# Performance work log

Hardware: AMD Instinct MI355X
Metric: run time of the kernel (lower is better)

The kernel has to match this reference:

```python
import jax, jax.numpy as jnp
from jax import lax
import numpy as np


def _fps(xyz, M):
    # Farthest point sampling: sequential over M steps, vectorized over batch.
    B, N, _ = xyz.shape
    def body(carry, _):
        dists, far = carry                       # dists:[B,N], far:[B]
        c = xyz[jnp.arange(B), far]              # [B,3] current centroid
        d = jnp.sum((xyz - c[:, None, :]) ** 2, axis=-1)
        dists = jnp.minimum(dists, d)
        nxt = jnp.argmax(dists, axis=-1).astype(jnp.int32)
        return (dists, nxt), far
    init = (jnp.full((B, N), 1e10, xyz.dtype), jnp.zeros((B,), jnp.int32))
    _, inds = lax.scan(body, init, None, length=M)
    return inds.T                                # [B, M]


def _ball_query(xyz, new_xyz, radius, K):
    # For each centroid pick first K point indices within radius; pad with first hit.
    N = xyz.shape[1]
    d2 = jnp.sum((new_xyz[:, :, None, :] - xyz[:, None, :, :]) ** 2, axis=-1)  # [B,M,N]
    ids = jnp.where(d2 <= radius * radius, jnp.arange(N)[None, None, :], N)
    ids = jnp.sort(ids, axis=-1)[..., :K]        # [B,M,K]
    return jnp.where(ids == N, ids[..., :1], ids)


_gather = jax.vmap(lambda p, i: p[i])            # p:[N,C], i:[M,K] -> [M,K,C]


def _mlp(x, layers):
    # Shared per-point MLP (1x1 conv + ReLU chain); BN omitted as in source head.
    for w, b in layers:
        x = jax.nn.relu(jnp.einsum('bmkc,cd->bmkd', x, w) + b)
    return x


def _sa(xyz, points, M, radius, K, layers):
    # Set-abstraction: FPS -> ball query -> group (centered xyz ++ feats) -> MLP -> max over K.
    fi = _fps(xyz, M)                                        # [B,M]
    new_xyz = jnp.take_along_axis(xyz, fi[..., None], axis=1)  # [B,M,3]
    gi = _ball_query(xyz, new_xyz, radius, K)                # [B,M,K]
    g_xyz = _gather(xyz, gi) - new_xyz[:, :, None, :]        # [B,M,K,3]
    g = jnp.concatenate([g_xyz, _gather(points, gi)], axis=-1)
    return new_xyz, jnp.max(_mlp(g, layers), axis=2)         # [B,M,Cout]


def _forward(xyz, points,
             w1a, b1a, w1b, b1b, w1c, b1c,
             w2a, b2a, w2b, b2b, w2c, b2c,
             w3a, b3a, w3b, b3b, w3c, b3c,
             lin1_w, lin2_w, cls_w, cls_b):
    B = xyz.shape[0]
    x1, f1 = _sa(xyz, points, 512, 0.2, 32, [(w1a, b1a), (w1b, b1b), (w1c, b1c)])
    x2, f2 = _sa(x1, f1, 128, 0.4, 64, [(w2a, b2a), (w2b, b2b), (w2c, b2c)])
    # group_all: single group containing all 128 points, feats = [xyz ++ points] (259 ch)
    g = jnp.concatenate([x2, f2], axis=-1)[:, None]           # [B,1,128,259]
    f3 = jnp.max(_mlp(g, [(w3a, b3a), (w3b, b3b), (w3c, b3c)]), axis=2)  # [B,1,1024]
    net = f3.reshape(B, -1)
    net = jax.nn.relu(net @ lin1_w)   # linear1 (no bias) + ReLU; dropout=identity (eval)
    net = jax.nn.relu(net @ lin2_w)
    return net @ cls_w + cls_b


def setup_inputs() -> dict:
    key = jax.random.key(0)
    ks = iter(jax.random.split(key, 40))
    B, N, NC = 32, 1024, 40
    inp = {}
    inp['xyz'] = jax.random.uniform(next(ks), (B, N, 3), jnp.float32, -1.0, 1.0)
    inp['points'] = jax.random.normal(next(ks), (B, N, 3), jnp.float32)
    def lin(cin, cout):
        w = jax.random.normal(next(ks), (cin, cout), jnp.float32) / np.float32(np.sqrt(cin))
        return w, jnp.zeros((cout,), jnp.float32)
    dims = {'1': [(6, 64), (64, 64), (64, 128)],
            '2': [(131, 128), (128, 128), (128, 256)],
            '3': [(259, 256), (256, 512), (512, 1024)]}
    for s, layer_dims in dims.items():
        for tag, (ci, co) in zip('abc', layer_dims):
            w, b = lin(ci, co)
            inp['w%s%s' % (s, tag)] = w
            inp['b%s%s' % (s, tag)] = b
    inp['lin1_w'] = jax.random.normal(next(ks), (1024, 512), jnp.float32) / np.float32(32.0)
    inp['lin2_w'] = jax.random.normal(next(ks), (512, 256), jnp.float32) / np.float32(np.sqrt(512))
    inp['cls_w'] = jax.random.normal(next(ks), (256, NC), jnp.float32) / np.float32(16.0)
    inp['cls_b'] = jnp.zeros((NC,), jnp.float32)
    return inp


def reference(xyz, points,
              w1a, b1a, w1b, b1b, w1c, b1c,
              w2a, b2a, w2b, b2b, w2c, b2c,
              w3a, b3a, w3b, b3b, w3c, b3c,
              lin1_w, lin2_w, cls_w, cls_b):
    return _forward(xyz, points,
                    w1a, b1a, w1b, b1b, w1c, b1c,
                    w2a, b2a, w2b, b2b, w2c, b2c,
                    w3a, b3a, w3b, b3b, w3c, b3c,
                    lin1_w, lin2_w, cls_w, cls_b)
```

## Files before the change

### kernel.cpp

```cpp
#include <hip/hip_runtime.h>

#define DEVFN __device__ __forceinline__

static inline int ceil_div(int a, int b) { return (a + b - 1) / b; }

typedef __attribute__((ext_vector_type(8))) short         bf16x8;
typedef __attribute__((ext_vector_type(4))) float         f32x4;
typedef __attribute__((ext_vector_type(8))) unsigned short u16x8;

DEVFN unsigned short f2bf(float x) {
    unsigned u = __float_as_uint(x);
    unsigned r = ((u >> 16) & 1u) + 0x7fffu;
    return (unsigned short)((u + r) >> 16);
}
DEVFN float bf2f(unsigned short h) { return __uint_as_float(((unsigned)h) << 16); }

template<int CTRL>
DEVFN double dpp_max_step(double v)
{
    int lo = __double2loint(v), hi = __double2hiint(v);
    int tlo = __builtin_amdgcn_update_dpp(lo, lo, CTRL, 0xF, 0xF, false);
    int thi = __builtin_amdgcn_update_dpp(hi, hi, CTRL, 0xF, 0xF, false);
    return fmax(v, __hiloint2double(thi, tlo));
}

template<int N>
__global__ __launch_bounds__(64) void fps_kernel(const float* __restrict__ xyz, int M,
                                                 int* __restrict__ out_idx,
                                                 float* __restrict__ nxout)
{
    constexpr int PPL = N / 64;
    int b = blockIdx.x, lane = threadIdx.x;
    __shared__ float4 sp[N];
    const float* p = xyz + (size_t)b * N * 3;
    float px[PPL], py[PPL], pz[PPL], dd[PPL];
    unsigned lo[PPL];
    #pragma unroll
    for (int j = 0; j < PPL; ++j) {
        int idx = lane + 64 * j;
        px[j] = p[idx*3+0]; py[j] = p[idx*3+1]; pz[j] = p[idx*3+2];
        sp[idx] = make_float4(px[j], py[j], pz[j], 0.f);
        dd[j] = 1e10f;
        lo[j] = ~(unsigned)idx;
    }
    __syncthreads();
    int far = 0;
    for (int s = 0; s < M; ++s) {
        float4 c4 = sp[far];
        if (lane == 0) {
            out_idx[(size_t)b*M + s] = far;
            nxout[((size_t)b*M + s)*3 + 0] = c4.x;
            nxout[((size_t)b*M + s)*3 + 1] = c4.y;
            nxout[((size_t)b*M + s)*3 + 2] = c4.z;
        }
        double cand[PPL];
        #pragma unroll
        for (int j = 0; j < PPL; ++j) {
            float dx = __fsub_rn(px[j], c4.x);
            float dy = __fsub_rn(py[j], c4.y);
            float dz = __fsub_rn(pz[j], c4.z);
            float d  = __fadd_rn(__fadd_rn(__fmul_rn(dx,dx), __fmul_rn(dy,dy)),
                                 __fmul_rn(dz,dz));
            float nd = fminf(dd[j], d);
            dd[j] = nd;
            cand[j] = __hiloint2double(__float_as_int(nd), (int)lo[j]);
        }
        #pragma unroll
        for (int st = PPL/2; st > 0; st >>= 1)
            #pragma unroll
            for (int j = 0; j < PPL; ++j)
                if (j < st) cand[j] = fmax(cand[j], cand[j + st]);
        double v = cand[0];
        v = dpp_max_step<0xB1>(v);
        v = dpp_max_step<0x4E>(v);
        v = dpp_max_step<0x124>(v);
        v = dpp_max_step<0x128>(v);
        v = dpp_max_step<0x142>(v);
        v = dpp_max_step<0x143>(v);
        int wlo = __builtin_amdgcn_readlane(__double2loint(v), 63);
        far = (int)(~(unsigned)wlo);
    }
}

__global__ void ballquery_kernel(const float* __restrict__ xyz,
                                 const float* __restrict__ new_xyz,
                                 int* __restrict__ gi,
                                 int B, int N, int M, int K, float r2)
{
    int t = blockIdx.x * blockDim.x + threadIdx.x;
    if (t >= B * M) return;
    int b = t / M;
    const float* p = xyz + (size_t)b * N * 3;
    float cx = new_xyz[t*3+0], cy = new_xyz[t*3+1], cz = new_xyz[t*3+2];
    int* out = gi + (size_t)t * K;
    int cnt = 0, first = 0;
    bool havefirst = false;
    for (int i = 0; i < N; ++i) {
        float dx = __fsub_rn(p[i*3+0], cx);
        float dy = __fsub_rn(p[i*3+1], cy);
        float dz = __fsub_rn(p[i*3+2], cz);
        float d  = __fadd_rn(__fadd_rn(__fmul_rn(dx,dx), __fmul_rn(dy,dy)),
                             __fmul_rn(dz,dz));
        if (d <= r2) {
            if (!havefirst) { first = i; havefirst = true; }
            out[cnt++] = i;
            if (cnt == K) break;
        }
    }
    for (; cnt < K; ++cnt) out[cnt] = first;
}

DEVFN float f4_elem(const float4& v, int u) {
    return u == 0 ? v.x : u == 1 ? v.y : u == 2 ? v.z : v.w;
}

__global__ void wsplit_kernel(const float* __restrict__ w,
                              unsigned short* __restrict__ wh,
                              unsigned short* __restrict__ wl,
                              int CItot, int CO, int CIpad, int ro)
{
    int t = blockIdx.x * 256 + threadIdx.x;
    if (t >= CIpad * CO) return;
    int co = t / CIpad, ci = t % CIpad;
    int src = ci + ro;
    float v = (src < CItot) ? w[(size_t)src * CO + co] : 0.f;
    unsigned short h = f2bf(v);
    wh[t] = h;
    wl[t] = f2bf(v - bf2f(h));
}

template<int CF, int CO, int KPTS>
__global__ __launch_bounds__(256) void sa_l1_kernel(
    const float* __restrict__ xyz, const float* __restrict__ feats,
    const float* __restrict__ new_xyz, const int* __restrict__ gi,
    const float* __restrict__ w, const float* __restrict__ bias,
    unsigned short* __restrict__ oh, unsigned short* __restrict__ ol,
    int N, int M, int row0)
{
    constexpr int WCH = CO / 4;
    const int lane = threadIdx.x & 63;
    const int wv   = __builtin_amdgcn_readfirstlane(threadIdx.x >> 6);
    const int rl   = blockIdx.x * 64 + lane;
    const int row  = row0 + rl;
    const int cent = row / KPTS;
    const int b    = cent / M;
    const int idx  = gi[row];
    const float* pp  = xyz + ((size_t)b*N + idx)*3;
    const float* cc3 = new_xyz + (size_t)cent*3;
    float a0 = __fsub_rn(pp[0], cc3[0]);
    float a1 = __fsub_rn(pp[1], cc3[1]);
    float a2 = __fsub_rn(pp[2], cc3[2]);
    const float* frow = feats + ((size_t)b*N + idx)*CF;
    const float* wcol = w + wv*WCH;
    const float* bcol = bias + wv*WCH;
    float acc[WCH];
    #pragma unroll
    for (int j = 0; j < WCH; ++j) acc[j] = bcol[j];
    #pragma unroll
    for (int j = 0; j < WCH; ++j) acc[j] += a0 * wcol[0*CO + j];
    #pragma unroll
    for (int j = 0; j < WCH; ++j) acc[j] += a1 * wcol[1*CO + j];
    #pragma unroll
    for (int j = 0; j < WCH; ++j) acc[j] += a2 * wcol[2*CO + j];
    constexpr int CF4 = CF & ~3;
    #pragma unroll 2
    for (int cc = 0; cc < CF4; cc += 4) {
        float4 a4 = *(const float4*)(frow + cc);
        #pragma unroll
        for (int u = 0; u < 4; ++u) {
            float a = f4_elem(a4, u);
            #pragma unroll
            for (int j = 0; j < WCH; ++j)
                acc[j] += a * wcol[(size_t)(3 + cc + u)*CO + j];
        }
    }
    #pragma unroll
    for (int f = CF4; f < CF; ++f) {
        float a = frow[f];
        #pragma unroll
        for (int j = 0; j < WCH; ++j)
            acc[j] += a * wcol[(size_t)(3 + f)*CO + j];
    }
    #pragma unroll
    for (int j8 = 0; j8 < WCH; j8 += 8) {
        u16x8 hv, lv;
        #pragma unroll
        for (int u = 0; u < 8; ++u) {
            float v = fmaxf(acc[j8+u], 0.f);
            unsigned short h = f2bf(v);
            hv[u] = (unsigned short)h;
            lv[u] = f2bf(v - bf2f(h));
        }
        size_t o = (size_t)rl*CO + wv*WCH + j8;
        *(u16x8*)(&oh[o]) = hv;
        *(u16x8*)(&ol[o]) = lv;
    }
}

template<int CI, int CO, int NTILE, int MROW, int KPTS, int OUTMODE>
__global__ __launch_bounds__(256) void mfma_layer_kernel(
    const unsigned short* __restrict__ ah, const unsigned short* __restrict__ al,
    const unsigned short* __restrict__ wh, const unsigned short* __restrict__ wl,
    const float* __restrict__ bias,
    unsigned short* __restrict__ oh, unsigned short* __restrict__ ol,
    float* __restrict__ ofp, int rowbase)
{
    constexpr int KT = CI / 32;
    static_assert(KT * MROW <= 18, "A-preload register budget");
    __shared__ float partial[4][OUTMODE >= 2 ? MROW : 1][OUTMODE >= 2 ? 16*NTILE : 1];
    const int wid  = threadIdx.x >> 6;
    const int lane = threadIdx.x & 63;
    const int m    = lane & 15;
    const int kg   = lane >> 4;
    const int blockrow = blockIdx.x * (64 * MROW);
    const int colbase  = blockIdx.y * (16 * NTILE);
    bf16x8 Ahf[MROW * KT], Alf[MROW * KT];
    #pragma unroll
    for (int t = 0; t < MROW; ++t) {
        const unsigned short* arh =
            ah + (size_t)(blockrow + t*64 + wid*16 + m) * CI + kg * 8;
        const unsigned short* arl =
            al + (size_t)(blockrow + t*64 + wid*16 + m) * CI + kg * 8;
        #pragma unroll
        for (int kt = 0; kt < KT; ++kt) {
            Ahf[t*KT + kt] = *(const bf16x8*)(arh + kt*32);
            Alf[t*KT + kt] = *(const bf16x8*)(arl + kt*32);
        }
    }
    #pragma unroll
    for (int nt = 0; nt < NTILE; ++nt) {
        f32x4 acc[MROW];
        #pragma unroll
        for (int t = 0; t < MROW; ++t) acc[t] = (f32x4){0.f, 0.f, 0.f, 0.f};
        const unsigned short* wbh = wh + (size_t)(colbase + nt*16 + m) * CI + kg * 8;
        const unsigned short* wbl = wl + (size_t)(colbase + nt*16 + m) * CI + kg * 8;
        #pragma unroll
        for (int kt = 0; kt < KT; ++kt) {
            bf16x8 Bh = *(const bf16x8*)(wbh + kt*32);
            bf16x8 Bl = *(const bf16x8*)(wbl + kt*32);
            #pragma unroll
            for (int t = 0; t < MROW; ++t) {
                acc[t] = __builtin_amdgcn_mfma_f32_16x16x32_bf16(Ahf[t*KT+kt], Bh, acc[t], 0, 0, 0);
                acc[t] = __builtin_amdgcn_mfma_f32_16x16x32_bf16(Ahf[t*KT+kt], Bl, acc[t], 0, 0, 0);
                acc[t] = __builtin_amdgcn_mfma_f32_16x16x32_bf16(Alf[t*KT+kt], Bh, acc[t], 0, 0, 0);
            }
        }
        int dcol = colbase + nt*16 + m;
        float bv = bias[dcol];
        #pragma unroll
        for (int t = 0; t < MROW; ++t) {
            float v[4];
            #pragma unroll
            for (int r = 0; r < 4; ++r) v[r] = fmaxf(acc[t][r] + bv, 0.f);
            if constexpr (OUTMODE == 0) {
                #pragma unroll
                for (int r = 0; r < 4; ++r) {
                    size_t o = (size_t)(blockrow + t*64 + wid*16 + kg*4 + r) * CO + dcol;
                    unsigned short h = f2bf(v[r]);
                    oh[o] = h;
                    ol[o] = f2bf(v[r] - bf2f(h));
                }
            } else if constexpr (OUTMODE == 1) {
                #pragma unroll
                for (int r = 0; r < 4; ++r)
                    ofp[(size_t)(blockrow + t*64 + wid*16 + kg*4 + r) * CO + dcol] = v[r];
            } else {
                float mx = fmaxf(fmaxf(v[0], v[1]), fmaxf(v[2], v[3]));
                mx = fmaxf(mx, __shfl_xor(mx, 16));
                mx = fmaxf(mx, __shfl_xor(mx, 32));
                if (lane < 16) partial[wid][t][nt*16 + m] = mx;
            }
        }
    }
    if constexpr (OUTMODE >= 2) {
        __syncthreads();
        for (int c = threadIdx.x; c < 16*NTILE; c += 256) {
            #pragma unroll
            for (int t = 0; t < MROW; ++t) {
                if constexpr (KPTS == 64) {
                    float mx = fmaxf(fmaxf(partial[0][t][c], partial[1][t][c]),
                                     fmaxf(partial[2][t][c], partial[3][t][c]));
                    int cent = (rowbase + blockrow) / 64 + t;
                    if constexpr (OUTMODE == 2) {
                        ofp[(size_t)cent*CO + colbase + c] = mx;
                    } else {
                        size_t o = (size_t)cent*CO + colbase + c;
                        unsigned short h = f2bf(mx);
                        oh[o] = h; ol[o] = f2bf(mx - bf2f(h));
                    }
                } else {
                    int cent0 = (rowbase + blockrow) / 32 + t*2;
                    float v0 = fmaxf(partial[0][t][c], partial[1][t][c]);
                    float v1 = fmaxf(partial[2][t][c], partial[3][t][c]);
                    if constexpr (OUTMODE == 2) {
                        ofp[(size_t)cent0*CO + colbase + c]     = v0;
                        ofp[(size_t)(cent0+1)*CO + colbase + c] = v1;
                    } else {
                        size_t o0 = (size_t)cent0*CO + colbase + c;
                        size_t o1 = (size_t)(cent0+1)*CO + colbase + c;
                        unsigned short h0 = f2bf(v0), h1 = f2bf(v1);
                        oh[o0] = h0; ol[o0] = f2bf(v0 - bf2f(h0));
                        oh[o1] = h1; ol[o1] = f2bf(v1 - bf2f(h1));
                    }
                }
            }
        }
    }
}

template<int NTILE, int MROW>
__global__ __launch_bounds__(256) void mfma_sa2l1_kernel(
    const float* __restrict__ sxyz,
    const float* __restrict__ cxyz,
    const int* __restrict__ gi,
    const unsigned short* __restrict__ f1h, const unsigned short* __restrict__ f1l,
    const float* __restrict__ w,
    const unsigned short* __restrict__ wh, const unsigned short* __restrict__ wl,
    const float* __restrict__ bias,
    unsigned short* __restrict__ oh, unsigned short* __restrict__ ol,
    int rowbase)
{
    constexpr int CI = 128, CO = 128, KT = 4, KPTS = 64, M = 128, N = 512;
    const int wid  = threadIdx.x >> 6;
    const int lane = threadIdx.x & 63;
    const int m    = lane & 15;
    const int kg   = lane >> 4;
    const int blockrow = blockIdx.x * (64 * MROW);
    const int colbase  = blockIdx.y * (16 * NTILE);
    bf16x8 Ahf[MROW * KT], Alf[MROW * KT];
    #pragma unroll
    for (int t = 0; t < MROW; ++t) {
        int grow = rowbase + blockrow + t*64 + wid*16 + m;
        int cent = grow / KPTS;
        int b    = cent / M;
        int idx  = gi[grow];
        const unsigned short* arh = f1h + ((size_t)b*N + idx) * CI + kg * 8;
        const unsigned short* arl = f1l + ((size_t)b*N + idx) * CI + kg * 8;
        #pragma unroll
        for (int kt = 0; kt < KT; ++kt) {
            Ahf[t*KT + kt] = *(const bf16x8*)(arh + kt*32);
            Alf[t*KT + kt] = *(const bf16x8*)(arl + kt*32);
        }
    }
    float dx[MROW][4], dy[MROW][4], dz[MROW][4];
    #pragma unroll
    for (int t = 0; t < MROW; ++t)
        #pragma unroll
        for (int r = 0; r < 4; ++r) {
            int grow = rowbase + blockrow + t*64 + wid*16 + kg*4 + r;
            int cent = grow / KPTS;
            int b    = cent / M;
            int idx  = gi[grow];
            const float* pp = sxyz + ((size_t)b*N + idx)*3;
            const float* cc = cxyz + (size_t)cent*3;
            dx[t][r] = __fsub_rn(pp[0], cc[0]);
            dy[t][r] = __fsub_rn(pp[1], cc[1]);
            dz[t][r] = __fsub_rn(pp[2], cc[2]);
        }
    #pragma unroll
    for (int nt = 0; nt < NTILE; ++nt) {
        f32x4 acc[MROW];
        #pragma unroll
        for (int t = 0; t < MROW; ++t) acc[t] = (f32x4){0.f, 0.f, 0.f, 0.f};
        const unsigned short* wbh = wh + (size_t)(colbase + nt*16 + m) * CI + kg * 8;
        const unsigned short* wbl = wl + (size_t)(colbase + nt*16 + m) * CI + kg * 8;
        #pragma unroll
        for (int kt = 0; kt < KT; ++kt) {
            bf16x8 Bh = *(const bf16x8*)(wbh + kt*32);
            bf16x8 Bl = *(const bf16x8*)(wbl + kt*32);
            #pragma unroll
            for (int t = 0; t < MROW; ++t) {
                acc[t] = __builtin_amdgcn_mfma_f32_16x16x32_bf16(Ahf[t*KT+kt], Bh, acc[t], 0, 0, 0);
                acc[t] = __builtin_amdgcn_mfma_f32_16x16x32_bf16(Ahf[t*KT+kt], Bl, acc[t], 0, 0, 0);
                acc[t] = __builtin_amdgcn_mfma_f32_16x16x32_bf16(Alf[t*KT+kt], Bh, acc[t], 0, 0, 0);
            }
        }
        int dcol = colbase + nt*16 + m;
        float w0 = w[0*CO + dcol], w1 = w[1*CO + dcol], w2 = w[2*CO + dcol];
        float bv = bias[dcol];
        #pragma unroll
        for (int t = 0; t < MROW; ++t)
            #pragma unroll
            for (int r = 0; r < 4; ++r) {
                float v = acc[t][r] + bv + dx[t][r]*w0 + dy[t][r]*w1 + dz[t][r]*w2;
                v = fmaxf(v, 0.f);
                size_t o = (size_t)(blockrow + t*64 + wid*16 + kg*4 + r) * CO + dcol;
                unsigned short h = f2bf(v);
                oh[o] = h;
                ol[o] = f2bf(v - bf2f(h));
            }
    }
}

__global__ void concat_split_kernel(const float* __restrict__ a, const float* __restrict__ f,
                                    unsigned short* __restrict__ oh,
                                    unsigned short* __restrict__ ol,
                                    int R, int CF, int CIpad)
{
    int t = blockIdx.x * 256 + threadIdx.x;
    if (t >= R * CIpad) return;
    int r = t / CIpad, c = t % CIpad;
    float v;
    if (c < 3) v = a[r*3 + c];
    else if (c < CF + 3) v = f[(size_t)r * CF + (c - 3)];
    else v = 0.f;
    unsigned short h = f2bf(v);
    oh[t] = h;
    ol[t] = f2bf(v - bf2f(h));
}

template<int RELU, int HASB>
__global__ __launch_bounds__(256) void fc_kernel(
    const float* __restrict__ A, const float* __restrict__ W,
    const float* __restrict__ bias, float* __restrict__ Cc,
    int Mr, int Nc, int Kd)
{
    int t = blockIdx.x * 256 + threadIdx.x;
    if (t >= Mr * Nc) return;
    int row = t / Nc, col = t % Nc;
    const float* a = A + (size_t)row * Kd;
    const float* w = W + col;
    float acc = 0.f;
    #pragma unroll 8
    for (int k = 0; k < Kd; ++k)
        acc += a[k] * w[(size_t)k * Nc];
    if (HASB) acc += bias[col];
    if (RELU) acc = fmaxf(acc, 0.f);
    Cc[t] = acc;
}

__global__ void rowmax_kernel(const float* __restrict__ in, float* __restrict__ out,
                              int B, int P, int C)
{
    int t = blockIdx.x * blockDim.x + threadIdx.x;
    if (t >= B * C) return;
    int b = t / C, c = t % C;
    const float* p = in + (size_t)b * P * C + c;
    float mx = p[0];
    for (int i = 1; i < P; ++i) mx = fmaxf(mx, p[(size_t)i * C]);
    out[t] = mx;
}

extern "C" void kernel_launch(void* const* d_in, const int* in_sizes, int n_in,
                              void* d_out, int out_size, void* d_ws, size_t ws_size,
                              hipStream_t stream)
{
    const float* xyz    = (const float*)d_in[0];
    const float* points = (const float*)d_in[1];
    const float* w1a = (const float*)d_in[2];  const float* b1a = (const float*)d_in[3];
    const float* w1b = (const float*)d_in[4];  const float* b1b = (const float*)d_in[5];
    const float* w1c = (const float*)d_in[6];  const float* b1c = (const float*)d_in[7];
    const float* w2a = (const float*)d_in[8];  const float* b2a = (const float*)d_in[9];
    const float* w2b = (const float*)d_in[10]; const float* b2b = (const float*)d_in[11];
    const float* w2c = (const float*)d_in[12]; const float* b2c = (const float*)d_in[13];
    const float* w3a = (const float*)d_in[14]; const float* b3a = (const float*)d_in[15];
    const float* w3b = (const float*)d_in[16]; const float* b3b = (const float*)d_in[17];
    const float* w3c = (const float*)d_in[18]; const float* b3c = (const float*)d_in[19];
    const float* lin1 = (const float*)d_in[20];
    const float* lin2 = (const float*)d_in[21];
    const float* clsw = (const float*)d_in[22];
    const float* clsb = (const float*)d_in[23];

    char* ws = (char*)d_ws;
    size_t off = 0;
    auto alloc = [&](size_t bytes) -> void* {
        void* p = ws + off;
        off += (bytes + 255) & ~(size_t)255;
        return p;
    };
    int*   fps1 = (int*)  alloc((size_t)32*512*4);
    float* nx1  = (float*)alloc((size_t)32*512*3*4);
    int*   gi1  = (int*)  alloc((size_t)32*512*32*4);
    int*   fps2 = (int*)  alloc((size_t)32*128*4);
    float* nx2  = (float*)alloc((size_t)32*128*3*4);
    int*   gi2  = (int*)  alloc((size_t)32*128*64*4);
    float* f2   = (float*)alloc((size_t)32*128*256*4);
    float* h3c  = (float*)alloc((size_t)4096*1024*4);
    float* f3   = (float*)alloc((size_t)32*1024*4);
    float* fc1  = (float*)alloc((size_t)32*512*4);
    float* fc2  = (float*)alloc((size_t)32*256*4);

    typedef unsigned short us;
    us* w1bh = (us*)alloc(64*64*2);     us* w1bl = (us*)alloc(64*64*2);
    us* w1ch = (us*)alloc(128*64*2);    us* w1cl = (us*)alloc(128*64*2);
    us* w2ah = (us*)alloc(128*128*2);   us* w2al = (us*)alloc(128*128*2);
    us* w2bh = (us*)alloc(128*128*2);   us* w2bl = (us*)alloc(128*128*2);
    us* w2ch = (us*)alloc(256*128*2);   us* w2cl = (us*)alloc(256*128*2);
    us* w3ah = (us*)alloc(256*288*2);   us* w3al = (us*)alloc(256*288*2);
    us* w3bh = (us*)alloc(512*256*2);   us* w3bl = (us*)alloc(512*256*2);
    us* w3ch = (us*)alloc(1024*512*2);  us* w3cl = (us*)alloc(1024*512*2);
    us* f1h  = (us*)alloc((size_t)16384*128*2);
    us* f1l  = (us*)alloc((size_t)16384*128*2);
    us* g3H  = (us*)alloc((size_t)4096*288*2);  us* g3L  = (us*)alloc((size_t)4096*288*2);
    us* h3aH = (us*)alloc((size_t)4096*256*2);  us* h3aL = (us*)alloc((size_t)4096*256*2);
    us* h3bH = (us*)alloc((size_t)4096*512*2);  us* h3bL = (us*)alloc((size_t)4096*512*2);

    size_t avail = (ws_size > off + 1024) ? (ws_size - off - 1024) : 0;
    size_t bufcap = avail / 4;
    if (bufcap > (size_t)67200000) bufcap = 67200000;
    us* Ah = (us*)alloc(bufcap); us* Al = (us*)alloc(bufcap);
    us* Bh = (us*)alloc(bufcap); us* Bl = (us*)alloc(bufcap);

    auto wsp = [&](const float* w, int CItot, int CO, int CIpad, int ro, us* wh, us* wl) {
        wsplit_kernel<<<ceil_div(CIpad*CO, 256), 256, 0, stream>>>(w, wh, wl, CItot, CO, CIpad, ro);
    };
    wsp(w1b, 64, 64, 64, 0,   w1bh, w1bl);
    wsp(w1c, 64, 128, 64, 0,  w1ch, w1cl);
    wsp(w2a, 131, 128, 128, 3, w2ah, w2al);
    wsp(w2b, 128, 128, 128, 0, w2bh, w2bl);
    wsp(w2c, 128, 256, 128, 0, w2ch, w2cl);
    wsp(w3a, 259, 256, 288, 0, w3ah, w3al);
    wsp(w3b, 256, 512, 256, 0, w3bh, w3bl);
    wsp(w3c, 512, 1024, 512, 0, w3ch, w3cl);

    fps_kernel<1024><<<32, 64, 0, stream>>>(xyz, 512, fps1, nx1);
    ballquery_kernel<<<ceil_div(32*512, 256), 256, 0, stream>>>(
        xyz, nx1, gi1, 32, 1024, 512, 32, (float)(0.2*0.2));
    {
        const int rows = 32*512*32;
        int ch = (int)((bufcap / (64*2)) & ~(size_t)1023);
        if (ch > rows) ch = rows;
        if (ch < 1024) ch = 1024;
        for (int r0 = 0; r0 < rows; r0 += ch) {
            int rc = rows - r0 < ch ? rows - r0 : ch;
            sa_l1_kernel<3, 64, 32><<<rc/64, 256, 0, stream>>>(
                xyz, points, nx1, gi1, w1a, b1a, Ah, Al, 1024, 512, r0);
            mfma_layer_kernel<64, 64, 4, 4, 0, 0><<<dim3(rc/256, 1), 256, 0, stream>>>(
                Ah, Al, w1bh, w1bl, b1b, Bh, Bl, nullptr, 0);
            mfma_layer_kernel<64, 128, 8, 4, 32, 3><<<dim3(rc/256, 1), 256, 0, stream>>>(
                Bh, Bl, w1ch, w1cl, b1c, f1h, f1l, nullptr, r0);
        }
    }

    fps_kernel<512><<<32, 64, 0, stream>>>(nx1, 128, fps2, nx2);
    ballquery_kernel<<<ceil_div(32*128, 256), 256, 0, stream>>>(
        nx1, nx2, gi2, 32, 512, 128, 64, (float)(0.4*0.4));
    {
        const int rows = 32*128*64;
        int ch = (int)((bufcap / (128*2)) & ~(size_t)1023);
        if (ch > rows) ch = rows;
        if (ch < 1024) ch = 1024;
        for (int r0 = 0; r0 < rows; r0 += ch) {
            int rc = rows - r0 < ch ? rows - r0 : ch;
            mfma_sa2l1_kernel<8, 2><<<dim3(rc/128, 1), 256, 0, stream>>>(
                nx1, nx2, gi2, f1h, f1l, w2a, w2ah, w2al, b2a, Ah, Al, r0);
            mfma_layer_kernel<128, 128, 8, 4, 0, 0><<<dim3(rc/256, 1), 256, 0, stream>>>(
                Ah, Al, w2bh, w2bl, b2b, Bh, Bl, nullptr, 0);
            mfma_layer_kernel<128, 256, 16, 4, 64, 2><<<dim3(rc/256, 1), 256, 0, stream>>>(
                Bh, Bl, w2ch, w2cl, b2c, nullptr, nullptr, f2, r0);
        }
    }

    concat_split_kernel<<<ceil_div(4096*288, 256), 256, 0, stream>>>(
        nx2, f2, g3H, g3L, 4096, 256, 288);
    mfma_layer_kernel<288, 256, 2, 1, 0, 0><<<dim3(4096/64, 256/32), 256, 0, stream>>>(
        g3H, g3L, w3ah, w3al, b3a, h3aH, h3aL, nullptr, 0);
    mfma_layer_kernel<256, 512, 2, 2, 0, 0><<<dim3(4096/128, 512/32), 256, 0, stream>>>(
        h3aH, h3aL, w3bh, w3bl, b3b, h3bH, h3bL, nullptr, 0);
    mfma_layer_kernel<512, 1024, 4, 1, 0, 1><<<dim3(4096/64, 1024/64), 256, 0, stream>>>(
        h3bH, h3bL, w3ch, w3cl, b3c, nullptr, nullptr, h3c, 0);
    rowmax_kernel<<<ceil_div(32*1024, 256), 256, 0, stream>>>(h3c, f3, 32, 128, 1024);

    fc_kernel<1,0><<<ceil_div(32*512, 256), 256, 0, stream>>>(
        f3, lin1, nullptr, fc1, 32, 512, 1024);
    fc_kernel<1,0><<<ceil_div(32*256, 256), 256, 0, stream>>>(
        fc1, lin2, nullptr, fc2, 32, 256, 512);
    fc_kernel<0,1><<<ceil_div(32*40, 256), 256, 0, stream>>>(
        fc2, clsw, clsb, (float*)d_out, 32, 40, 256);
}
```

Before: 1.262 ms.

## Fuse each set-abstraction MLP chain into one kernel with LDS intermediates

Replaces the three-kernel-per-chunk pipelines for SA1 and SA2 (layer1, layer2, layer3+max) with single fused kernels per stage. Each block holds one or two centroids' grouped rows, keeps the intermediate activations as hi/lo bf16 in LDS, and performs the max-over-K reduction in-block before writing features. This removes the large global round-trips of intermediate activations and the extra launches. In exchange it uses more LDS per block, which may lower occupancy, and weights are re-read per block rather than amortised over larger row tiles.

Measured after the change: 1.414 ms. 1.12x slower.

```diff
diff --git a/kernel.cpp b/kernel.cpp
--- a/kernel.cpp
+++ b/kernel.cpp
@@ -7,13 +7,14 @@
 typedef __attribute__((ext_vector_type(8))) short         bf16x8;
 typedef __attribute__((ext_vector_type(4))) float         f32x4;
 typedef __attribute__((ext_vector_type(8))) unsigned short u16x8;
-
-DEVFN unsigned short f2bf(float x) {
+typedef unsigned short us;
+
+DEVFN us f2bf(float x) {
     unsigned u = __float_as_uint(x);
     unsigned r = ((u >> 16) & 1u) + 0x7fffu;
-    return (unsigned short)((u + r) >> 16);
-}
-DEVFN float bf2f(unsigned short h) { return __uint_as_float(((unsigned)h) << 16); }
+    return (us)((u + r) >> 16);
+}
+DEVFN float bf2f(us h) { return __uint_as_float(((unsigned)h) << 16); }
 
 template<int CTRL>
 DEVFN double dpp_max_step(double v)
@@ -110,13 +111,8 @@
     for (; cnt < K; ++cnt) out[cnt] = first;
 }
 
-DEVFN float f4_elem(const float4& v, int u) {
-    return u == 0 ? v.x : u == 1 ? v.y : u == 2 ? v.z : v.w;
-}
-
 __global__ void wsplit_kernel(const float* __restrict__ w,
-                              unsigned short* __restrict__ wh,
-                              unsigned short* __restrict__ wl,
+                              us* __restrict__ wh, us* __restrict__ wl,
                               int CItot, int CO, int CIpad, int ro)
 {
     int t = blockIdx.x * 256 + threadIdx.x;
@@ -124,90 +120,303 @@
     int co = t / CIpad, ci = t % CIpad;
     int src = ci + ro;
     float v = (src < CItot) ? w[(size_t)src * CO + co] : 0.f;
-    unsigned short h = f2bf(v);
+    us h = f2bf(v);
     wh[t] = h;
     wl[t] = f2bf(v - bf2f(h));
 }
 
-template<int CF, int CO, int KPTS>
-__global__ __launch_bounds__(256) void sa_l1_kernel(
+__global__ __launch_bounds__(256) void sa1_fused_kernel(
     const float* __restrict__ xyz, const float* __restrict__ feats,
     const float* __restrict__ new_xyz, const int* __restrict__ gi,
-    const float* __restrict__ w, const float* __restrict__ bias,
-    unsigned short* __restrict__ oh, unsigned short* __restrict__ ol,
-    int N, int M, int row0)
-{
-    constexpr int WCH = CO / 4;
+    const float* __restrict__ w1a, const float* __restrict__ b1a,
+    const us* __restrict__ w1bh, const us* __restrict__ w1bl, const float* __restrict__ b1b,
+    const us* __restrict__ w1ch, const us* __restrict__ w1cl, const float* __restrict__ b1c,
+    us* __restrict__ f1h, us* __restrict__ f1l)
+{
+    constexpr int N = 1024, M = 512, KPTS = 32, PAD = 88;
+    __shared__ __align__(16) us l1h[64*PAD], l1l[64*PAD];
+    __shared__ __align__(16) us l2h[64*PAD], l2l[64*PAD];
+    __shared__ float partial[4][128];
     const int lane = threadIdx.x & 63;
-    const int wv   = __builtin_amdgcn_readfirstlane(threadIdx.x >> 6);
-    const int rl   = blockIdx.x * 64 + lane;
-    const int row  = row0 + rl;
-    const int cent = row / KPTS;
+    const int wid  = threadIdx.x >> 6;
+    const int m    = lane & 15;
+    const int kg   = lane >> 4;
+
+    {
+        const int row  = blockIdx.x * 64 + lane;
+        const int cent = row / KPTS;
+        const int b    = cent / M;
+        const int idx  = gi[row];
+        const float* pp  = xyz + ((size_t)b*N + idx)*3;
+        const float* cc3 = new_xyz + (size_t)cent*3;
+        float a0 = __fsub_rn(pp[0], cc3[0]);
+        float a1 = __fsub_rn(pp[1], cc3[1]);
+        float a2 = __fsub_rn(pp[2], cc3[2]);
+        const float* frow = feats + ((size_t)b*N + idx)*3;
+        float f0 = frow[0], f1v = frow[1], f2v = frow[2];
+        const float* wcol = w1a + wid*16;
+        const float* bcol = b1a + wid*16;
+        float acc[16];
+        #pragma unroll
+        for (int j = 0; j < 16; ++j) {
+            float a = bcol[j];
+            a += a0 * wcol[0*64 + j];
+            a += a1 * wcol[1*64 + j];
+            a += a2 * wcol[2*64 + j];
+            a += f0 * wcol[3*64 + j];
+            a += f1v * wcol[4*64 + j];
+            a += f2v * wcol[5*64 + j];
+            acc[j] = a;
+        }
+        #pragma unroll
+        for (int j8 = 0; j8 < 16; j8 += 8) {
+            u16x8 hv, lv;
+            #pragma unroll
+            for (int u = 0; u < 8; ++u) {
+                float v = fmaxf(acc[j8+u], 0.f);
+                us h = f2bf(v);
+                hv[u] = h;
+                lv[u] = f2bf(v - bf2f(h));
+            }
+            *(u16x8*)&l1h[lane*PAD + wid*16 + j8] = hv;
+            *(u16x8*)&l1l[lane*PAD + wid*16 + j8] = lv;
+        }
+    }
+    __syncthreads();
+
+    {
+        bf16x8 Ahf[2], Alf[2];
+        #pragma unroll
+        for (int kt = 0; kt < 2; ++kt) {
+            Ahf[kt] = *(const bf16x8*)&l1h[(wid*16 + m)*PAD + kt*32 + kg*8];
+            Alf[kt] = *(const bf16x8*)&l1l[(wid*16 + m)*PAD + kt*32 + kg*8];
+        }
+        #pragma unroll
+        for (int nt = 0; nt < 4; ++nt) {
+            f32x4 acc = {0.f, 0.f, 0.f, 0.f};
+            const us* wbh = w1bh + (size_t)(nt*16 + m)*64 + kg*8;
+            const us* wbl = w1bl + (size_t)(nt*16 + m)*64 + kg*8;
+            #pragma unroll
+            for (int kt = 0; kt < 2; ++kt) {
+                bf16x8 Bh = *(const bf16x8*)(wbh + kt*32);
+                bf16x8 Bl = *(const bf16x8*)(wbl + kt*32);
+                acc = __builtin_amdgcn_mfma_f32_16x16x32_bf16(Ahf[kt], Bh, acc, 0, 0, 0);
+                acc = __builtin_amdgcn_mfma_f32_16x16x32_bf16(Ahf[kt], Bl, acc, 0, 0, 0);
+                acc = __builtin_amdgcn_mfma_f32_16x16x32_bf16(Alf[kt], Bh, acc, 0, 0, 0);
+            }
+            int dcol = nt*16 + m;
+            float bv = b1b[dcol];
+            #pragma unroll
+            for (int r = 0; r < 4; ++r) {
+                float v = fmaxf(acc[r] + bv, 0.f);
+                us h = f2bf(v);
+                l2h[(wid*16 + kg*4 + r)*PAD + dcol] = h;
+                l2l[(wid*16 + kg*4 + r)*PAD + dcol] = f2bf(v - bf2f(h));
+            }
+        }
+    }
+    __syncthreads();
+
+    {
+        bf16x8 Ahf[2], Alf[2];
+        #pragma unroll
+        for (int kt = 0; kt < 2; ++kt) {
+            Ahf[kt] = *(const bf16x8*)&l2h[(wid*16 + m)*PAD + kt*32 + kg*8];
+            Alf[kt] = *(const bf16x8*)&l2l[(wid*16 + m)*PAD + kt*32 + kg*8];
+        }
+        #pragma unroll
+        for (int nt = 0; nt < 8; ++nt) {
+            f32x4 acc = {0.f, 0.f, 0.f, 0.f};
+            const us* wbh = w1ch + (size_t)(nt*16 + m)*64 + kg*8;
+            const us* wbl = w1cl + (size_t)(nt*16 + m)*64 + kg*8;
+            #pragma unroll
+            for (int kt = 0; kt < 2; ++kt) {
+                bf16x8 Bh = *(const bf16x8*)(wbh + kt*32);
+                bf16x8 Bl = *(const bf16x8*)(wbl + kt*32);
+                acc = __builtin_amdgcn_mfma_f32_16x16x32_bf16(Ahf[kt], Bh, acc, 0, 0, 0);
+                acc = __builtin_amdgcn_mfma_f32_16x16x32_bf16(Ahf[kt], Bl, acc, 0, 0, 0);
+                acc = __builtin_amdgcn_mfma_f32_16x16x32_bf16(Alf[kt], Bh, acc, 0, 0, 0);
+            }
+            int dcol = nt*16 + m;
+            float bv = b1c[dcol];
+            float v0 = fmaxf(acc[0] + bv, 0.f);
+            float v1 = fmaxf(acc[1] + bv, 0.f);
+            float v2 = fmaxf(acc[2] + bv, 0.f);
+            float v3 = fmaxf(acc[3] + bv, 0.f);
+            float mx = fmaxf(fmaxf(v0, v1), fmaxf(v2, v3));
+            mx = fmaxf(mx, __shfl_xor(mx, 16));
+            mx = fmaxf(mx, __shfl_xor(mx, 32));
+            if (lane < 16) partial[wid][dcol] = mx;
+        }
+    }
+    __syncthreads();
+    for (int c = threadIdx.x; c < 128; c += 256) {
+        float v0 = fmaxf(partial[0][c], partial[1][c]);
+        float v1 = fmaxf(partial[2][c], partial[3][c]);
+        int cent0 = blockIdx.x * 2;
+        size_t o0 = (size_t)cent0*128 + c;
+        size_t o1 = (size_t)(cent0+1)*128 + c;
+        us h0 = f2bf(v0), h1 = f2bf(v1);
+        f1h[o0] = h0; f1l[o0] = f2bf(v0 - bf2f(h0));
+        f1h[o1] = h1; f1l[o1] = f2bf(v1 - bf2f(h1));
+    }
+}
+
+__global__ __launch_bounds__(256) void sa2_fused_kernel(
+    const float* __restrict__ sxyz, const float* __restrict__ cxyz,
+    const int* __restrict__ gi,
+    const us* __restrict__ f1h, const us* __restrict__ f1l,
+    const float* __restrict__ w2a,
+    const us* __restrict__ w2ah, const us* __restrict__ w2al, const float* __restrict__ b2a,
+    const us* __restrict__ w2bh, const us* __restrict__ w2bl, const float* __restrict__ b2b,
+    const us* __restrict__ w2ch, const us* __restrict__ w2cl, const float* __restrict__ b2c,
+    float* __restrict__ f2)
+{
+    constexpr int M = 128, N = 512, PAD = 136;
+    __shared__ __align__(16) us l1h[64*PAD], l1l[64*PAD];
+    __shared__ __align__(16) us l2h[64*PAD], l2l[64*PAD];
+    __shared__ float partial[4][256];
+    const int lane = threadIdx.x & 63;
+    const int wid  = threadIdx.x >> 6;
+    const int m    = lane & 15;
+    const int kg   = lane >> 4;
+    const int cent = blockIdx.x;
     const int b    = cent / M;
-    const int idx  = gi[row];
-    const float* pp  = xyz + ((size_t)b*N + idx)*3;
-    const float* cc3 = new_xyz + (size_t)cent*3;
-    float a0 = __fsub_rn(pp[0], cc3[0]);
-    float a1 = __fsub_rn(pp[1], cc3[1]);
-    float a2 = __fsub_rn(pp[2], cc3[2]);
-    const float* frow = feats + ((size_t)b*N + idx)*CF;
-    const float* wcol = w + wv*WCH;
-    const float* bcol = bias + wv*WCH;
-    float acc[WCH];
-    #pragma unroll
-    for (int j = 0; j < WCH; ++j) acc[j] = bcol[j];
-    #pragma unroll
-    for (int j = 0; j < WCH; ++j) acc[j] += a0 * wcol[0*CO + j];
-    #pragma unroll
-    for (int j = 0; j < WCH; ++j) acc[j] += a1 * wcol[1*CO + j];
-    #pragma unroll
-    for (int j = 0; j < WCH; ++j) acc[j] += a2 * wcol[2*CO + j];
-    constexpr int CF4 = CF & ~3;
-    #pragma unroll 2
-    for (int cc = 0; cc < CF4; cc += 4) {
-        float4 a4 = *(const float4*)(frow + cc);
-        #pragma unroll
-        for (int u = 0; u < 4; ++u) {
-            float a = f4_elem(a4, u);
-            #pragma unroll
-            for (int j = 0; j < WCH; ++j)
-                acc[j] += a * wcol[(size_t)(3 + cc + u)*CO + j];
-        }
-    }
-    #pragma unroll
-    for (int f = CF4; f < CF; ++f) {
-        float a = frow[f];
-        #pragma unroll
-        for (int j = 0; j < WCH; ++j)
-            acc[j] += a * wcol[(size_t)(3 + f)*CO + j];
-    }
-    #pragma unroll
-    for (int j8 = 0; j8 < WCH; j8 += 8) {
-        u16x8 hv, lv;
-        #pragma unroll
-        for (int u = 0; u < 8; ++u) {
-            float v = fmaxf(acc[j8+u], 0.f);
-            unsigned short h = f2bf(v);
-            hv[u] = (unsigned short)h;
-            lv[u] = f2bf(v - bf2f(h));
-        }
-        size_t o = (size_t)rl*CO + wv*WCH + j8;
-        *(u16x8*)(&oh[o]) = hv;
-        *(u16x8*)(&ol[o]) = lv;
-    }
-}
-
-template<int CI, int CO, int NTILE, int MROW, int KPTS, int OUTMODE>
+
+    {
+        bf16x8 Ahf[4], Alf[4];
+        {
+            int grow = cent*64 + wid*16 + m;
+            int idx  = gi[grow];
+            const us* arh = f1h + ((size_t)b*N + idx) * 128 + kg*8;
+            const us* arl = f1l + ((size_t)b*N + idx) * 128 + kg*8;
+            #pragma unroll
+            for (int kt = 0; kt < 4; ++kt) {
+                Ahf[kt] = *(const bf16x8*)(arh + kt*32);
+                Alf[kt] = *(const bf16x8*)(arl + kt*32);
+            }
+        }
+        float dx[4], dy[4], dz[4];
+        #pragma unroll
+        for (int r = 0; r < 4; ++r) {
+            int grow = cent*64 + wid*16 + kg*4 + r;
+            int idx  = gi[grow];
+            const float* pp = sxyz + ((size_t)b*N + idx)*3;
+            const float* cc = cxyz + (size_t)cent*3;
+            dx[r] = __fsub_rn(pp[0], cc[0]);
+            dy[r] = __fsub_rn(pp[1], cc[1]);
+            dz[r] = __fsub_rn(pp[2], cc[2]);
+        }
+        #pragma unroll
+        for (int nt = 0; nt < 8; ++nt) {
+            f32x4 acc = {0.f, 0.f, 0.f, 0.f};
+            const us* wbh = w2ah + (size_t)(nt*16 + m)*128 + kg*8;
+            const us* wbl = w2al + (size_t)(nt*16 + m)*128 + kg*8;
+            #pragma unroll
+            for (int kt = 0; kt < 4; ++kt) {
+                bf16x8 Bh = *(const bf16x8*)(wbh + kt*32);
+                bf16x8 Bl = *(const bf16x8*)(wbl + kt*32);
+                acc = __builtin_amdgcn_mfma_f32_16x16x32_bf16(Ahf[kt], Bh, acc, 0, 0, 0);
+                acc = __builtin_amdgcn_mfma_f32_16x16x32_bf16(Ahf[kt], Bl, acc, 0, 0, 0);
+                acc = __builtin_amdgcn_mfma_f32_16x16x32_bf16(Alf[kt], Bh, acc, 0, 0, 0);
+            }
+            int dcol = nt*16 + m;
+            float w0 = w2a[0*128 + dcol], w1 = w2a[1*128 + dcol], w2 = w2a[2*128 + dcol];
+            float bv = b2a[dcol];
+            #pragma unroll
+            for (int r = 0; r < 4; ++r) {
+                float v = acc[r] + bv + dx[r]*w0 + dy[r]*w1 + dz[r]*w2;
+                v = fmaxf(v, 0.f);
+                us h = f2bf(v);
+                l1h[(wid*16 + kg*4 + r)*PAD + dcol] = h;
+                l1l[(wid*16 + kg*4 + r)*PAD + dcol] = f2bf(v - bf2f(h));
+            }
+        }
+    }
+    __syncthreads();
+
+    {
+        bf16x8 Ahf[4], Alf[4];
+        #pragma unroll
+        for (int kt = 0; kt < 4; ++kt) {
+            Ahf[kt] = *(const bf16x8*)&l1h[(wid*16 + m)*PAD + kt*32 + kg*8];
+            Alf[kt] = *(const bf16x8*)&l1l[(wid*16 + m)*PAD + kt*32 + kg*8];
+        }
+        #pragma unroll
+        for (int nt = 0; nt < 8; ++nt) {
+            f32x4 acc = {0.f, 0.f, 0.f, 0.f};
+            const us* wbh = w2bh + (size_t)(nt*16 + m)*128 + kg*8;
+            const us* wbl = w2bl + (size_t)(nt*16 + m)*128 + kg*8;
+            #pragma unroll
+            for (int kt = 0; kt < 4; ++kt) {
+                bf16x8 Bh = *(const bf16x8*)(wbh + kt*32);
+                bf16x8 Bl = *(const bf16x8*)(wbl + kt*32);
+                acc = __builtin_amdgcn_mfma_f32_16x16x32_bf16(Ahf[kt], Bh, acc, 0, 0, 0);
+                acc = __builtin_amdgcn_mfma_f32_16x16x32_bf16(Ahf[kt], Bl, acc, 0, 0, 0);
+                acc = __builtin_amdgcn_mfma_f32_16x16x32_bf16(Alf[kt], Bh, acc, 0, 0, 0);
+            }
+            int dcol = nt*16 + m;
+            float bv = b2b[dcol];
+            #pragma unroll
+            for (int r = 0; r < 4; ++r) {
+                float v = fmaxf(acc[r] + bv, 0.f);
+                us h = f2bf(v);
+                l2h[(wid*16 + kg*4 + r)*PAD + dcol] = h;
+                l2l[(wid*16 + kg*4 + r)*PAD + dcol] = f2bf(v - bf2f(h));
+            }
+        }
+    }
+    __syncthreads();
+
+    {
+        bf16x8 Ahf[4], Alf[4];
+        #pragma unroll
+        for (int kt = 0; kt < 4; ++kt) {
+            Ahf[kt] = *(const bf16x8*)&l2h[(wid*16 + m)*PAD + kt*32 + kg*8];
+            Alf[kt] = *(const bf16x8*)&l2l[(wid*16 + m)*PAD + kt*32 + kg*8];
+        }
+        #pragma unroll
+        for (int nt = 0; nt < 16; ++nt) {
+            f32x4 acc = {0.f, 0.f, 0.f, 0.f};
+            const us* wbh = w2ch + (size_t)(nt*16 + m)*128 + kg*8;
+            const us* wbl = w2cl + (size_t)(nt*16 + m)*128 + kg*8;
+            #pragma unroll
+            for (int kt = 0; kt < 4; ++kt) {
+                bf16x8 Bh = *(const bf16x8*)(wbh + kt*32);
+                bf16x8 Bl = *(const bf16x8*)(wbl + kt*32);
+                acc = __builtin_amdgcn_mfma_f32_16x16x32_bf16(Ahf[kt], Bh, acc, 0, 0, 0);
+                acc = __builtin_amdgcn_mfma_f32_16x16x32_bf16(Ahf[kt], Bl, acc, 0, 0, 0);
+                acc = __builtin_amdgcn_mfma_f32_16x16x32_bf16(Alf[kt], Bh, acc, 0, 0, 0);
+            }
+            int dcol = nt*16 + m;
+            float bv = b2c[dcol];
+            float v0 = fmaxf(acc[0] + bv, 0.f);
+            float v1 = fmaxf(acc[1] + bv, 0.f);
+            float v2 = fmaxf(acc[2] + bv, 0.f);
+            float v3 = fmaxf(acc[3] + bv, 0.f);
+            float mx = fmaxf(fmaxf(v0, v1), fmaxf(v2, v3));
+            mx = fmaxf(mx, __shfl_xor(mx, 16));
+            mx = fmaxf(mx, __shfl_xor(mx, 32));
+            if (lane < 16) partial[wid][dcol] = mx;
+        }
+    }
+    __syncthreads();
+    for (int c = threadIdx.x; c < 256; c += 256) {
+        float mx = fmaxf(fmaxf(partial[0][c], partial[1][c]),
+                         fmaxf(partial[2][c], partial[3][c]));
+        f2[(size_t)cent*256 + c] = mx;
+    }
+}
+
+template<int CI, int CO, int NTILE, int MROW, int OUTMODE>
 __global__ __launch_bounds__(256) void mfma_layer_kernel(
-    const unsigned short* __restrict__ ah, const unsigned short* __restrict__ al,
-    const unsigned short* __restrict__ wh, const unsigned short* __restrict__ wl,
+    const us* __restrict__ ah, const us* __restrict__ al,
+    const us* __restrict__ wh, const us* __restrict__ wl,
     const float* __restrict__ bias,
-    unsigned short* __restrict__ oh, unsigned short* __restrict__ ol,
-    float* __restrict__ ofp, int rowbase)
+    us* __restrict__ oh, us* __restrict__ ol, float* __restrict__ ofp)
 {
     constexpr int KT = CI / 32;
     static_assert(KT * MROW <= 18, "A-preload register budget");
-    __shared__ float partial[4][OUTMODE >= 2 ? MROW : 1][OUTMODE >= 2 ? 16*NTILE : 1];
     const int wid  = threadIdx.x >> 6;
     const int lane = threadIdx.x & 63;
     const int m    = lane & 15;
@@ -217,10 +426,8 @@
     bf16x8 Ahf[MROW * KT], Alf[MROW * KT];
     #pragma unroll
     for (int t = 0; t < MROW; ++t) {
-        const unsigned short* arh =
-            ah + (size_t)(blockrow + t*64 + wid*16 + m) * CI + kg * 8;
-        const unsigned short* arl =
-            al + (size_t)(blockrow + t*64 + wid*16 + m) * CI + kg * 8;
+        const us* arh = ah + (size_t)(blockrow + t*64 + wid*16 + m) * CI + kg * 8;
+        const us* arl = al + (size_t)(blockrow + t*64 + wid*16 + m) * CI + kg * 8;
         #pragma unroll
         for (int kt = 0; kt < KT; ++kt) {
             Ahf[t*KT + kt] = *(const bf16x8*)(arh + kt*32);
@@ -232,8 +439,8 @@
         f32x4 acc[MROW];
         #pragma unroll
         for (int t = 0; t < MROW; ++t) acc[t] = (f32x4){0.f, 0.f, 0.f, 0.f};
-        const unsigned short* wbh = wh + (size_t)(colbase + nt*16 + m) * CI + kg * 8;
-        const unsigned short* wbl = wl + (size_t)(colbase + nt*16 + m) * CI + kg * 8;
+        const us* wbh = wh + (size_t)(colbase + nt*16 + m) * CI + kg * 8;
+        const us* wbl = wl + (size_t)(colbase + nt*16 + m) * CI + kg * 8;
         #pragma unroll
         for (int kt = 0; kt < KT; ++kt) {
             bf16x8 Bh = *(const bf16x8*)(wbh + kt*32);
@@ -249,152 +456,24 @@
         float bv = bias[dcol];
         #pragma unroll
         for (int t = 0; t < MROW; ++t) {
-            float v[4];
-            #pragma unroll
-            for (int r = 0; r < 4; ++r) v[r] = fmaxf(acc[t][r] + bv, 0.f);
-            if constexpr (OUTMODE == 0) {
-                #pragma unroll
-                for (int r = 0; r < 4; ++r) {
-                    size_t o = (size_t)(blockrow + t*64 + wid*16 + kg*4 + r) * CO + dcol;
-                    unsigned short h = f2bf(v[r]);
+            #pragma unroll
+            for (int r = 0; r < 4; ++r) {
+                float v = fmaxf(acc[t][r] + bv, 0.f);
+                size_t o = (size_t)(blockrow + t*64 + wid*16 + kg*4 + r) * CO + dcol;
+                if constexpr (OUTMODE == 0) {
+                    us h = f2bf(v);
                     oh[o] = h;
-                    ol[o] = f2bf(v[r] - bf2f(h));
+                    ol[o] = f2bf(v - bf2f(h));
+                } else {
+                    ofp[o] = v;
                 }
-            } else if constexpr (OUTMODE == 1) {
-                #pragma unroll
-                for (int r = 0; r < 4; ++r)
-                    ofp[(size_t)(blockrow + t*64 + wid*16 + kg*4 + r) * CO + dcol] = v[r];
-            } else {
-                float mx = fmaxf(fmaxf(v[0], v[1]), fmaxf(v[2], v[3]));
-                mx = fmaxf(mx, __shfl_xor(mx, 16));
-                mx = fmaxf(mx, __shfl_xor(mx, 32));
-                if (lane < 16) partial[wid][t][nt*16 + m] = mx;
-            }
-        }
-    }
-    if constexpr (OUTMODE >= 2) {
-        __syncthreads();
-        for (int c = threadIdx.x; c < 16*NTILE; c += 256) {
-            #pragma unroll
-            for (int t = 0; t < MROW; ++t) {
-                if constexpr (KPTS == 64) {
-                    float mx = fmaxf(fmaxf(partial[0][t][c], partial[1][t][c]),
-                                     fmaxf(partial[2][t][c], partial[3][t][c]));
-                    int cent = (rowbase + blockrow) / 64 + t;
-                    if constexpr (OUTMODE == 2) {
-                        ofp[(size_t)cent*CO + colbase + c] = mx;
-                    } else {
-                        size_t o = (size_t)cent*CO + colbase + c;
-                        unsigned short h = f2bf(mx);
-                        oh[o] = h; ol[o] = f2bf(mx - bf2f(h));
-                    }
-                } else {
-                    int cent0 = (rowbase + blockrow) / 32 + t*2;
-                    float v0 = fmaxf(partial[0][t][c], partial[1][t][c]);
-                    float v1 = fmaxf(partial[2][t][c], partial[3][t][c]);
-                    if constexpr (OUTMODE == 2) {
-                        ofp[(size_t)cent0*CO + colbase + c]     = v0;
-                        ofp[(size_t)(cent0+1)*CO + colbase + c] = v1;
-                    } else {
-                        size_t o0 = (size_t)cent0*CO + colbase + c;
-                        size_t o1 = (size_t)(cent0+1)*CO + colbase + c;
-                        unsigned short h0 = f2bf(v0), h1 = f2bf(v1);
-                        oh[o0] = h0; ol[o0] = f2bf(v0 - bf2f(h0));
-                        oh[o1] = h1; ol[o1] = f2bf(v1 - bf2f(h1));
-                    }
-                }
-            }
-        }
-    }
-}
-
-template<int NTILE, int MROW>
-__global__ __launch_bounds__(256) void mfma_sa2l1_kernel(
-    const float* __restrict__ sxyz,
-    const float* __restrict__ cxyz,
-    const int* __restrict__ gi,
-    const unsigned short* __restrict__ f1h, const unsigned short* __restrict__ f1l,
-    const float* __restrict__ w,
-    const unsigned short* __restrict__ wh, const unsigned short* __restrict__ wl,
-    const float* __restrict__ bias,
-    unsigned short* __restrict__ oh, unsigned short* __restrict__ ol,
-    int rowbase)
-{
-    constexpr int CI = 128, CO = 128, KT = 4, KPTS = 64, M = 128, N = 512;
-    const int wid  = threadIdx.x >> 6;
-    const int lane = threadIdx.x & 63;
-    const int m    = lane & 15;
-    const int kg   = lane >> 4;
-    const int blockrow = blockIdx.x * (64 * MROW);
-    const int colbase  = blockIdx.y * (16 * NTILE);
-    bf16x8 Ahf[MROW * KT], Alf[MROW * KT];
-    #pragma unroll
-    for (int t = 0; t < MROW; ++t) {
-        int grow = rowbase + blockrow + t*64 + wid*16 + m;
-        int cent = grow / KPTS;
-        int b    = cent / M;
-        int idx  = gi[grow];
-        const unsigned short* arh = f1h + ((size_t)b*N + idx) * CI + kg * 8;
-        const unsigned short* arl = f1l + ((size_t)b*N + idx) * CI + kg * 8;
-        #pragma unroll
-        for (int kt = 0; kt < KT; ++kt) {
-            Ahf[t*KT + kt] = *(const bf16x8*)(arh + kt*32);
-            Alf[t*KT + kt] = *(const bf16x8*)(arl + kt*32);
-        }
-    }
-    float dx[MROW][4], dy[MROW][4], dz[MROW][4];
-    #pragma unroll
-    for (int t = 0; t < MROW; ++t)
-        #pragma unroll
-        for (int r = 0; r < 4; ++r) {
-            int grow = rowbase + blockrow + t*64 + wid*16 + kg*4 + r;
-            int cent = grow / KPTS;
-            int b    = cent / M;
-            int idx  = gi[grow];
-            const float* pp = sxyz + ((size_t)b*N + idx)*3;
-            const float* cc = cxyz + (size_t)cent*3;
-            dx[t][r] = __fsub_rn(pp[0], cc[0]);
-            dy[t][r] = __fsub_rn(pp[1], cc[1]);
-            dz[t][r] = __fsub_rn(pp[2], cc[2]);
-        }
-    #pragma unroll
-    for (int nt = 0; nt < NTILE; ++nt) {
-        f32x4 acc[MROW];
-        #pragma unroll
-        for (int t = 0; t < MROW; ++t) acc[t] = (f32x4){0.f, 0.f, 0.f, 0.f};
-        const unsigned short* wbh = wh + (size_t)(colbase + nt*16 + m) * CI + kg * 8;
-        const unsigned short* wbl = wl + (size_t)(colbase + nt*16 + m) * CI + kg * 8;
-        #pragma unroll
-        for (int kt = 0; kt < KT; ++kt) {
-            bf16x8 Bh = *(const bf16x8*)(wbh + kt*32);
-            bf16x8 Bl = *(const bf16x8*)(wbl + kt*32);
-            #pragma unroll
-            for (int t = 0; t < MROW; ++t) {
-                acc[t] = __builtin_amdgcn_mfma_f32_16x16x32_bf16(Ahf[t*KT+kt], Bh, acc[t], 0, 0, 0);
-                acc[t] = __builtin_amdgcn_mfma_f32_16x16x32_bf16(Ahf[t*KT+kt], Bl, acc[t], 0, 0, 0);
-                acc[t] = __builtin_amdgcn_mfma_f32_16x16x32_bf16(Alf[t*KT+kt], Bh, acc[t], 0, 0, 0);
-            }
-        }
-        int dcol = colbase + nt*16 + m;
-        float w0 = w[0*CO + dcol], w1 = w[1*CO + dcol], w2 = w[2*CO + dcol];
-        float bv = bias[dcol];
-        #pragma unroll
-        for (int t = 0; t < MROW; ++t)
-            #pragma unroll
-            for (int r = 0; r < 4; ++r) {
-                float v = acc[t][r] + bv + dx[t][r]*w0 + dy[t][r]*w1 + dz[t][r]*w2;
-                v = fmaxf(v, 0.f);
-                size_t o = (size_t)(blockrow + t*64 + wid*16 + kg*4 + r) * CO + dcol;
-                unsigned short h = f2bf(v);
-                oh[o] = h;
-                ol[o] = f2bf(v - bf2f(h));
-            }
+            }
+        }
     }
 }
 
 __global__ void concat_split_kernel(const float* __restrict__ a, const float* __restrict__ f,
-                                    unsigned short* __restrict__ oh,
-                                    unsigned short* __restrict__ ol,
+                                    us* __restrict__ oh, us* __restrict__ ol,
                                     int R, int CF, int CIpad)
 {
     int t = blockIdx.x * 256 + threadIdx.x;
@@ -404,7 +483,7 @@
     if (c < 3) v = a[r*3 + c];
     else if (c < CF + 3) v = f[(size_t)r * CF + (c - 3)];
     else v = 0.f;
-    unsigned short h = f2bf(v);
+    us h = f2bf(v);
     oh[t] = h;
     ol[t] = f2bf(v - bf2f(h));
 }
@@ -480,7 +559,6 @@
     float* fc1  = (float*)alloc((size_t)32*512*4);
     float* fc2  = (float*)alloc((size_t)32*256*4);
 
-    typedef unsigned short us;
     us* w1bh = (us*)alloc(64*64*2);     us* w1bl = (us*)alloc(64*64*2);
     us* w1ch = (us*)alloc(128*64*2);    us* w1cl = (us*)alloc(128*64*2);
     us* w2ah = (us*)alloc(128*128*2);   us* w2al = (us*)alloc(128*128*2);
@@ -495,12 +573,6 @@
     us* h3aH = (us*)alloc((size_t)4096*256*2);  us* h3aL = (us*)alloc((size_t)4096*256*2);
     us* h3bH = (us*)alloc((size_t)4096*512*2);  us* h3bL = (us*)alloc((size_t)4096*512*2);
 
-    size_t avail = (ws_size > off + 1024) ? (ws_size - off - 1024) : 0;
-    size_t bufcap = avail / 4;
-    if (bufcap > (size_t)67200000) bufcap = 67200000;
-    us* Ah = (us*)alloc(bufcap); us* Al = (us*)alloc(bufcap);
-    us* Bh = (us*)alloc(bufcap); us* Bl = (us*)alloc(bufcap);
-
     auto wsp = [&](const float* w, int CItot, int CO, int CIpad, int ro, us* wh, us* wl) {
         wsplit_kernel<<<ceil_div(CIpad*CO, 256), 256, 0, stream>>>(w, wh, wl, CItot, CO, CIpad, ro);
     };
@@ -516,49 +588,24 @@
     fps_kernel<1024><<<32, 64, 0, stream>>>(xyz, 512, fps1, nx1);
     ballquery_kernel<<<ceil_div(32*512, 256), 256, 0, stream>>>(
         xyz, nx1, gi1, 32, 1024, 512, 32, (float)(0.2*0.2));
-    {
-        const int rows = 32*512*32;
-        int ch = (int)((bufcap / (64*2)) & ~(size_t)1023);
-        if (ch > rows) ch = rows;
-        if (ch < 1024) ch = 1024;
-        for (int r0 = 0; r0 < rows; r0 += ch) {
-            int rc = rows - r0 < ch ? rows - r0 : ch;
-            sa_l1_kernel<3, 64, 32><<<rc/64, 256, 0, stream>>>(
-                xyz, points, nx1, gi1, w1a, b1a, Ah, Al, 1024, 512, r0);
-            mfma_layer_kernel<64, 64, 4, 4, 0, 0><<<dim3(rc/256, 1), 256, 0, stream>>>(
-                Ah, Al, w1bh, w1bl, b1b, Bh, Bl, nullptr, 0);
-            mfma_layer_kernel<64, 128, 8, 4, 32, 3><<<dim3(rc/256, 1), 256, 0, stream>>>(
-                Bh, Bl, w1ch, w1cl, b1c, f1h, f1l, nullptr, r0);
-        }
-    }
+    sa1_fused_kernel<<<32*512*32/64, 256, 0, stream>>>(
+        xyz, points, nx1, gi1, w1a, b1a, w1bh, w1bl, b1b, w1ch, w1cl, b1c, f1h, f1l);
 
     fps_kernel<512><<<32, 64, 0, stream>>>(nx1, 128, fps2, nx2);
     ballquery_kernel<<<ceil_div(32*128, 256), 256, 0, stream>>>(
         nx1, nx2, gi2, 32, 512, 128, 64, (float)(0.4*0.4));
-    {
-        const int rows = 32*128*64;
-        int ch = (int)((bufcap / (128*2)) & ~(size_t)1023);
-        if (ch > rows) ch = rows;
-        if (ch < 1024) ch = 1024;
-        for (int r0 = 0; r0 < rows; r0 += ch) {
-            int rc = rows - r0 < ch ? rows - r0 : ch;
-            mfma_sa2l1_kernel<8, 2><<<dim3(rc/128, 1), 256, 0, stream>>>(
-                nx1, nx2, gi2, f1h, f1l, w2a, w2ah, w2al, b2a, Ah, Al, r0);
-            mfma_layer_kernel<128, 128, 8, 4, 0, 0><<<dim3(rc/256, 1), 256, 0, stream>>>(
-                Ah, Al, w2bh, w2bl, b2b, Bh, Bl, nullptr, 0);
-            mfma_layer_kernel<128, 256, 16, 4, 64, 2><<<dim3(rc/256, 1), 256, 0, stream>>>(
-                Bh, Bl, w2ch, w2cl, b2c, nullptr, nullptr, f2, r0);
-        }
-    }
+    sa2_fused_kernel<<<32*128, 256, 0, stream>>>(
+        nx1, nx2, gi2, f1h, f1l, w2a, w2ah, w2al, b2a,
+        w2bh, w2bl, b2b, w2ch, w2cl, b2c, f2);
 
     concat_split_kernel<<<ceil_div(4096*288, 256), 256, 0, stream>>>(
         nx2, f2, g3H, g3L, 4096, 256, 288);
-    mfma_layer_kernel<288, 256, 2, 1, 0, 0><<<dim3(4096/64, 256/32), 256, 0, stream>>>(
-        g3H, g3L, w3ah, w3al, b3a, h3aH, h3aL, nullptr, 0);
-    mfma_layer_kernel<256, 512, 2, 2, 0, 0><<<dim3(4096/128, 512/32), 256, 0, stream>>>(
-        h3aH, h3aL, w3bh, w3bl, b3b, h3bH, h3bL, nullptr, 0);
-    mfma_layer_kernel<512, 1024, 4, 1, 0, 1><<<dim3(4096/64, 1024/64), 256, 0, stream>>>(
-        h3bH, h3bL, w3ch, w3cl, b3c, nullptr, nullptr, h3c, 0);
+    mfma_layer_kernel<288, 256, 2, 1, 0><<<dim3(4096/64, 256/32), 256, 0, stream>>>(
+        g3H, g3L, w3ah, w3al, b3a, h3aH, h3aL, nullptr);
+    mfma_layer_kernel<256, 512, 2, 2, 0><<<dim3(4096/128, 512/32), 256, 0, stream>>>(
+        h3aH, h3aL, w3bh, w3bl, b3b, h3bH, h3bL, nullptr);
+    mfma_layer_kernel<512, 1024, 4, 1, 1><<<dim3(4096/64, 1024/64), 256, 0, stream>>>(
+        h3bH, h3bL, w3ch, w3cl, b3c, nullptr, nullptr, h3c);
     rowmax_kernel<<<ceil_div(32*1024, 256), 256, 0, stream>>>(h3c, f3, 32, 128, 1024);
 
     fc_kernel<1,0><<<ceil_div(32*512, 256), 256, 0, stream>>>(
```
